# Performance work log

Measured on AMD Instinct MI355X. Metric: run time of the kernel, lower is better.

## Reference

```python
import jax, jax.numpy as jnp
import numpy as np

N_NODES = 100000
N_EDGES = 1600000
DIM_IN, DIM_H, DIM_OUT = 500, 64, 8


def setup_inputs() -> dict:
    key = jax.random.key(0)
    k_x, k_e, k_w1, k_w2 = jax.random.split(key, 4)
    x = jax.random.normal(k_x, (N_NODES, DIM_IN), dtype=jnp.float32)
    edge_index = jax.random.randint(k_e, (2, N_EDGES), 0, N_NODES, dtype=jnp.int32)
    # Glorot-ish init for linear weights, zero bias (PyG GCNConv default)
    W1 = jax.random.normal(k_w1, (DIM_IN, DIM_H), dtype=jnp.float32) * (1.0 / np.sqrt(DIM_IN))
    b1 = jnp.zeros((DIM_H,), dtype=jnp.float32)
    W2 = jax.random.normal(k_w2, (DIM_H, DIM_OUT), dtype=jnp.float32) * (1.0 / np.sqrt(DIM_H))
    b2 = jnp.zeros((DIM_OUT,), dtype=jnp.float32)
    return {"x": x, "edge_index": edge_index, "W1": W1, "b1": b1, "W2": W2, "b2": b2}


def _gcn_conv(h, W, b, src, dst, edge_norm, num_nodes):
    """GCNConv: out = D^{-1/2}(A+I)D^{-1/2} (h W) + b, via gather/scatter over edges."""
    hw = h @ W                                  # [N, d_out] dense transform
    msg = hw[src] * edge_norm[:, None]          # [E+N, d_out] gather + scale
    agg = jax.ops.segment_sum(msg, dst, num_segments=num_nodes)  # scatter-add
    return agg + b


def reference(x, edge_index, W1, b1, W2, b2):
    num_nodes = x.shape[0]
    # Add self-loops (PyG GCNConv default: add_self_loops=True)
    loops = jnp.arange(num_nodes, dtype=edge_index.dtype)
    src = jnp.concatenate([edge_index[0], loops])
    dst = jnp.concatenate([edge_index[1], loops])
    # Symmetric normalization from in-degree of loop-augmented graph
    deg = jax.ops.segment_sum(jnp.ones_like(dst, dtype=x.dtype), dst,
                              num_segments=num_nodes)
    dinv = jnp.where(deg > 0, jax.lax.rsqrt(deg), 0.0)
    edge_norm = dinv[src] * dinv[dst]           # [E+N]
    # Eval-mode forward (dropout is identity when not training)
    h = jax.nn.relu(_gcn_conv(x, W1, b1, src, dst, edge_norm, num_nodes))
    h = _gcn_conv(h, W2, b2, src, dst, edge_norm, num_nodes)
    return jax.nn.log_softmax(h, axis=1)
```

## Files before the change

kernel.cpp:

```cpp
#include <hip/hip_runtime.h>
#include <stdint.h>

#define NN 100000
#define NE 1600000
#define DIN 500
#define DH 64
#define DOUT 8
#define KP 512
#define MAXDEG 64

#define FILL_EPT 4
#define FILL_PASSES 16
#define FILL_RS ((NN + FILL_PASSES - 1) / FILL_PASSES)

typedef __attribute__((ext_vector_type(8))) short short8;
typedef __attribute__((ext_vector_type(4))) float f32x4;
typedef unsigned short ushort_t;

static __device__ __forceinline__ ushort_t f2bf(float f) {
  union { float f; uint32_t u; } v; v.f = f;
  uint32_t u = v.u;
  return (ushort_t)((u + 0x7FFFu + ((u >> 16) & 1u)) >> 16);
}
static __device__ __forceinline__ float bf2f(ushort_t h) {
  union { uint32_t u; float f; } v; v.u = ((uint32_t)h) << 16;
  return v.f;
}

static __device__ __forceinline__ void gload16(const void* g, void* l) {
  __builtin_amdgcn_global_load_lds((const __attribute__((address_space(1))) uint32_t*)g,
                                   (__attribute__((address_space(3))) uint32_t*)l, 16, 0, 0);
}

__global__ __launch_bounds__(256) void k_fill(const int* __restrict__ ei,
                                              int* __restrict__ cursor,
                                              int* __restrict__ colsrc) {
  int t = blockIdx.x * 256 + threadIdx.x;
  const int T = gridDim.x * 256;
  int s[FILL_EPT], d[FILL_EPT];
#pragma unroll
  for (int k = 0; k < FILL_EPT; ++k) {
    int id = t + k * T;
    s[k] = 0; d[k] = -1;
    if (id < NE) { s[k] = ei[id]; d[k] = ei[NE + id]; }
    else if (id < NE + NN) { s[k] = id - NE; d[k] = s[k]; }
  }
#pragma unroll 1
  for (int p = 0; p < FILL_PASSES; ++p) {
    int lo = p * FILL_RS;
    int hi = lo + FILL_RS;
#pragma unroll
    for (int k = 0; k < FILL_EPT; ++k) {
      bool act = (d[k] >= lo) && (d[k] < hi);
      if (__any(act)) {
        if (act) {
          int pos = atomicAdd(&cursor[d[k]], 1);
          if (pos < MAXDEG) colsrc[d[k] * MAXDEG + pos] = s[k];
        }
      }
    }
  }
}

__global__ __launch_bounds__(256) void k_dinv(const int* __restrict__ cursor,
                                              float* __restrict__ dinv) {
  int v = blockIdx.x * 256 + threadIdx.x;
  if (v >= NN) return;
  dinv[v] = 1.0f / sqrtf((float)cursor[v]);
}

__global__ __launch_bounds__(256) void k_w1cvt(const float* __restrict__ W1,
                                               ushort_t* __restrict__ bt) {
  int id = blockIdx.x * 256 + threadIdx.x;
  if (id >= DH * KP * 2) return;
  int i = id & 7, lane = (id >> 3) & 63, h = (id >> 9) & 1;
  int off = (id >> 10) & 3, kkg = id >> 12;
  int r = lane & 15, g = lane >> 4;
  int col = off * 16 + r;
  int k = kkg * 32 + g * 8 + i;
  float v = (k < DIN) ? W1[k * DH + col] : 0.0f;
  ushort_t hi = f2bf(v);
  bt[id] = h ? f2bf(v - bf2f(hi)) : hi;
}

__global__ __launch_bounds__(256) void k_gemm1(const float* __restrict__ x,
                                               const ushort_t* __restrict__ bt,
                                               ushort_t* __restrict__ hwb) {
  __shared__ float lds[2][64 * 128];
  int tid = threadIdx.x;
  int lane = tid & 63, w = tid >> 6;
  int r = lane & 15, g = lane >> 4;
  int row0 = blockIdx.x * 64;

  auto stage = [&](int ch, int b) {
    float* base = &lds[b][0];
#pragma unroll
    for (int j = 0; j < 8; ++j) {
      int idx = j * 256 + tid;
      int row = idx >> 5;
      int q   = idx & 31;
      int qd  = q ^ (row & 7);
      int kq  = ch * 32 + qd;
      if (kq > 124) kq = 124;
      int grow = row0 + row;
      if (grow >= NN) grow = NN - 1;
      gload16(x + (size_t)grow * DIN + kq * 4, base + idx * 4);
    }
  };

  f32x4 acc0 = {0,0,0,0}, acc1 = {0,0,0,0}, acc2 = {0,0,0,0}, acc3 = {0,0,0,0};
  int rowl = w * 16 + r;
  int sw = rowl & 7;

  stage(0, 0);
  __syncthreads();
#pragma unroll 1
  for (int ch = 0; ch < 4; ++ch) {
    if (ch < 3) stage(ch + 1, (ch + 1) & 1);
    __builtin_amdgcn_sched_barrier(0);
#pragma unroll
    for (int kk = 0; kk < 4; ++kk) {
      int q0 = kk * 8 + g * 2;
      f32x4 v0 = *(const f32x4*)(&lds[ch & 1][rowl * 128 + ((q0)     ^ sw) * 4]);
      f32x4 v1 = *(const f32x4*)(&lds[ch & 1][rowl * 128 + ((q0 + 1) ^ sw) * 4]);
      float a[8] = {v0.x, v0.y, v0.z, v0.w, v1.x, v1.y, v1.z, v1.w};
      short8 ah, al;
#pragma unroll
      for (int i = 0; i < 8; ++i) {
        ushort_t hi = f2bf(a[i]);
        ah[i] = (short)hi;
        al[i] = (short)f2bf(a[i] - bf2f(hi));
      }
      int kkg = ch * 4 + kk;
      const ushort_t* bph = bt + (size_t)(kkg * 4 * 2) * 512 + lane * 8;
#define TILE(T, OFF)                                                            \
      {                                                                         \
        short8 bhf = *(const short8*)(bph + (OFF) * 2 * 512);                   \
        short8 blf = *(const short8*)(bph + ((OFF) * 2 + 1) * 512);             \
        T = __builtin_amdgcn_mfma_f32_16x16x32_bf16(ah, bhf, T, 0, 0, 0);       \
        T = __builtin_amdgcn_mfma_f32_16x16x32_bf16(al, bhf, T, 0, 0, 0);       \
        T = __builtin_amdgcn_mfma_f32_16x16x32_bf16(ah, blf, T, 0, 0, 0);       \
      }
      TILE(acc0, 0) TILE(acc1, 1) TILE(acc2, 2) TILE(acc3, 3)
#undef TILE
    }
    __syncthreads();
  }
  int wrow0 = row0 + w * 16;
#pragma unroll
  for (int i = 0; i < 4; ++i) {
    int orow = wrow0 + g * 4 + i;
    if (orow < NN) {
      ushort_t* o = hwb + (size_t)orow * DH + r;
      o[0]  = f2bf(acc0[i]);
      o[16] = f2bf(acc1[i]);
      o[32] = f2bf(acc2[i]);
      o[48] = f2bf(acc3[i]);
    }
  }
}

__global__ __launch_bounds__(256) void k_agg1(const ushort_t* __restrict__ hwb,
                                              const int* __restrict__ colsrc,
                                              const int* __restrict__ cnt,
                                              const float* __restrict__ dinv,
                                              const float* __restrict__ b1,
                                              const float* __restrict__ W2,
                                              float* __restrict__ hw2) {
  int lane = threadIdx.x & 63;
  int v = blockIdx.x * 4 + (threadIdx.x >> 6);
  if (v >= NN) return;
  int c = cnt[v]; if (c > MAXDEG) c = MAXDEG;
  float dv = dinv[v];
  const int* cl = colsrc + v * MAXDEG;
  int si = cl[lane];
  bool act = lane < c;
  if (!act) si = 0;
  float nrmv = act ? dinv[si] * dv : 0.0f;
  float acc = 0.0f;
  for (int i0 = 0; i0 < c; i0 += 16) {
    float val[16];
#pragma unroll
    for (int j = 0; j < 16; ++j) {
      int s = __builtin_amdgcn_readlane(si, i0 + j);
      val[j] = bf2f(hwb[(size_t)s * DH + lane]);
    }
#pragma unroll
    for (int j = 0; j < 16; ++j) {
      float nrm = __uint_as_float(__builtin_amdgcn_readlane(__float_as_uint(nrmv), i0 + j));
      acc = fmaf(val[j], nrm, acc);
    }
  }
  float h = acc + b1[lane];
  h = h > 0.0f ? h : 0.0f;
  const float* w2r = W2 + lane * DOUT;
  float p0 = h * w2r[0], p1 = h * w2r[1], p2 = h * w2r[2], p3 = h * w2r[3];
  float p4 = h * w2r[4], p5 = h * w2r[5], p6 = h * w2r[6], p7 = h * w2r[7];
#pragma unroll
  for (int off = 32; off > 0; off >>= 1) {
    p0 += __shfl_xor(p0, off); p1 += __shfl_xor(p1, off);
    p2 += __shfl_xor(p2, off); p3 += __shfl_xor(p3, off);
    p4 += __shfl_xor(p4, off); p5 += __shfl_xor(p5, off);
    p6 += __shfl_xor(p6, off); p7 += __shfl_xor(p7, off);
  }
  if (lane == 0) {
    float4 q0 = {p0, p1, p2, p3}, q1 = {p4, p5, p6, p7};
    *(float4*)(hw2 + (size_t)v * DOUT)     = q0;
    *(float4*)(hw2 + (size_t)v * DOUT + 4) = q1;
  }
}

__global__ __launch_bounds__(256) void k_agg2(const float* __restrict__ hw2,
                                              const int* __restrict__ colsrc,
                                              const int* __restrict__ cnt,
                                              const float* __restrict__ dinv,
                                              const float* __restrict__ b2,
                                              float* __restrict__ out) {
  int lane = threadIdx.x & 63;
  int v = blockIdx.x * 4 + (threadIdx.x >> 6);
  if (v >= NN) return;
  int e = lane >> 3, f = lane & 7;
  int c = cnt[v]; if (c > MAXDEG) c = MAXDEG;
  float dv = dinv[v];
  const int* cl = colsrc + v * MAXDEG;
  float acc = 0.0f;
  for (int i0 = 0; i0 < c; i0 += 8) {
    int i = i0 + e;
    bool a2 = i < c;
    int s = a2 ? cl[i] : 0;
    float nrm = a2 ? dinv[s] * dv : 0.0f;
    float val = hw2[(size_t)s * DOUT + f] * nrm;
    val += __shfl_xor(val, 8);
    val += __shfl_xor(val, 16);
    val += __shfl_xor(val, 32);
    acc += val;
  }
  acc += b2[f];
  float m = acc;
  m = fmaxf(m, __shfl_xor(m, 1));
  m = fmaxf(m, __shfl_xor(m, 2));
  m = fmaxf(m, __shfl_xor(m, 4));
  float ex = expf(acc - m);
  float sum = ex;
  sum += __shfl_xor(sum, 1);
  sum += __shfl_xor(sum, 2);
  sum += __shfl_xor(sum, 4);
  float ls = m + logf(sum);
  if (e == 0) out[(size_t)v * DOUT + f] = acc - ls;
}

extern "C" void kernel_launch(void* const* d_in, const int* in_sizes, int n_in,
                              void* d_out, int out_size, void* d_ws, size_t ws_size,
                              hipStream_t stream) {
  const float* x  = (const float*)d_in[0];
  const int*   ei = (const int*)d_in[1];
  const float* W1 = (const float*)d_in[2];
  const float* b1 = (const float*)d_in[3];
  const float* W2 = (const float*)d_in[4];
  const float* b2 = (const float*)d_in[5];
  float* out = (float*)d_out;

  char* w = (char*)d_ws;
  size_t off = 0;
  auto alloc = [&](size_t bytes) {
    char* p = w + off;
    off += (bytes + 255) & ~(size_t)255;
    return (void*)p;
  };
  int*      cursor = (int*)alloc((size_t)NN * 4);
  float*    dinv   = (float*)alloc((size_t)NN * 4);
  ushort_t* bt     = (ushort_t*)alloc((size_t)DH * KP * 2 * 2);
  int*      colsrc = (int*)alloc((size_t)NN * MAXDEG * 4);
  ushort_t* hwb    = (ushort_t*)alloc((size_t)NN * DH * 2);
  float*    hw2    = (float*)alloc((size_t)NN * DOUT * 4);

  hipMemsetAsync(cursor, 0, (size_t)NN * 4, stream);
  int fill_blocks = (NE + NN + 256 * FILL_EPT - 1) / (256 * FILL_EPT);
  k_fill<<<fill_blocks, 256, 0, stream>>>(ei, cursor, colsrc);
  k_dinv<<<(NN + 255) / 256, 256, 0, stream>>>(cursor, dinv);
  k_w1cvt<<<(DH * KP * 2 + 255) / 256, 256, 0, stream>>>(W1, bt);
  k_gemm1<<<(NN + 63) / 64, 256, 0, stream>>>(x, bt, hwb);
  k_agg1<<<(NN + 3) / 4, 256, 0, stream>>>(hwb, colsrc, cursor, dinv, b1, W2, hw2);
  k_agg2<<<(NN + 3) / 4, 256, 0, stream>>>(hw2, colsrc, cursor, dinv, b2, out);
}
```

Before: 286.7 us.

## Fuse CSR fill and GEMM1 into one interleaved kernel, prefetch B fragments

Merges the atomic-based CSR fill and the first dense GEMM into one launch whose blocks alternate between fill and GEMM roles, so the latency-bound scatter atomics overlap with the bandwidth/MFMA-bound GEMM. The GEMM now double-buffers the W1 bf16 fragments in registers ahead of each MFMA step and drops the LDS XOR swizzle. It also adds nontemporal loads for edges and a nontemporal output store. Risks include more LDS bank conflicts without the swizzle, higher register pressure from 16 short8 buffers, and fill blocks reserving the full LDS allocation.

```diff
diff --git a/kernel.cpp b/kernel.cpp
--- a/kernel.cpp
+++ b/kernel.cpp
@@ -12,6 +12,8 @@
 #define FILL_EPT 4
 #define FILL_PASSES 16
 #define FILL_RS ((NN + FILL_PASSES - 1) / FILL_PASSES)
+#define GEMMB ((NN + 63) / 64)
+#define FILLB ((NE + NN + 256 * FILL_EPT - 1) / (256 * FILL_EPT))
 
 typedef __attribute__((ext_vector_type(8))) short short8;
 typedef __attribute__((ext_vector_type(4))) float f32x4;
@@ -30,36 +32,6 @@
 static __device__ __forceinline__ void gload16(const void* g, void* l) {
   __builtin_amdgcn_global_load_lds((const __attribute__((address_space(1))) uint32_t*)g,
                                    (__attribute__((address_space(3))) uint32_t*)l, 16, 0, 0);
-}
-
-__global__ __launch_bounds__(256) void k_fill(const int* __restrict__ ei,
-                                              int* __restrict__ cursor,
-                                              int* __restrict__ colsrc) {
-  int t = blockIdx.x * 256 + threadIdx.x;
-  const int T = gridDim.x * 256;
-  int s[FILL_EPT], d[FILL_EPT];
-#pragma unroll
-  for (int k = 0; k < FILL_EPT; ++k) {
-    int id = t + k * T;
-    s[k] = 0; d[k] = -1;
-    if (id < NE) { s[k] = ei[id]; d[k] = ei[NE + id]; }
-    else if (id < NE + NN) { s[k] = id - NE; d[k] = s[k]; }
-  }
-#pragma unroll 1
-  for (int p = 0; p < FILL_PASSES; ++p) {
-    int lo = p * FILL_RS;
-    int hi = lo + FILL_RS;
-#pragma unroll
-    for (int k = 0; k < FILL_EPT; ++k) {
-      bool act = (d[k] >= lo) && (d[k] < hi);
-      if (__any(act)) {
-        if (act) {
-          int pos = atomicAdd(&cursor[d[k]], 1);
-          if (pos < MAXDEG) colsrc[d[k] * MAXDEG + pos] = s[k];
-        }
-      }
-    }
-  }
 }
 
 __global__ __launch_bounds__(256) void k_dinv(const int* __restrict__ cursor,
@@ -83,67 +55,111 @@
   bt[id] = h ? f2bf(v - bf2f(hi)) : hi;
 }
 
-__global__ __launch_bounds__(256) void k_gemm1(const float* __restrict__ x,
+__global__ __launch_bounds__(256) void k_front(const int* __restrict__ ei,
+                                               int* __restrict__ cursor,
+                                               int* __restrict__ colsrc,
+                                               const float* __restrict__ x,
                                                const ushort_t* __restrict__ bt,
                                                ushort_t* __restrict__ hwb) {
   __shared__ float lds[2][64 * 128];
+  int bid = blockIdx.x;
   int tid = threadIdx.x;
+
+  int fid, gid;
+  if (bid < 2 * GEMMB) {
+    if ((bid & 1) == 0) { fid = bid >> 1; gid = -1; }
+    else                { gid = bid >> 1; fid = -1; }
+  } else { fid = GEMMB + (bid - 2 * GEMMB); gid = -1; }
+
+  if (fid >= 0) {
+    int t = fid * 256 + tid;
+    const int T = FILLB * 256;
+    int s[FILL_EPT], d[FILL_EPT];
+#pragma unroll
+    for (int k = 0; k < FILL_EPT; ++k) {
+      int id = t + k * T;
+      s[k] = 0; d[k] = -1;
+      if (id < NE) {
+        s[k] = __builtin_nontemporal_load(ei + id);
+        d[k] = __builtin_nontemporal_load(ei + NE + id);
+      } else if (id < NE + NN) { s[k] = id - NE; d[k] = s[k]; }
+    }
+#pragma unroll 1
+    for (int p = 0; p < FILL_PASSES; ++p) {
+      int lo = p * FILL_RS;
+      int hi = lo + FILL_RS;
+#pragma unroll
+      for (int k = 0; k < FILL_EPT; ++k) {
+        bool act = (d[k] >= lo) && (d[k] < hi);
+        if (__any(act)) {
+          if (act) {
+            int pos = atomicAdd(&cursor[d[k]], 1);
+            if (pos < MAXDEG) colsrc[d[k] * MAXDEG + pos] = s[k];
+          }
+        }
+      }
+    }
+    return;
+  }
+
   int lane = tid & 63, w = tid >> 6;
   int r = lane & 15, g = lane >> 4;
-  int row0 = blockIdx.x * 64;
+  int row0 = gid * 64;
+  int rowl = w * 16 + r;
 
   auto stage = [&](int ch, int b) {
     float* base = &lds[b][0];
 #pragma unroll
     for (int j = 0; j < 8; ++j) {
       int idx = j * 256 + tid;
-      int row = idx >> 5;
-      int q   = idx & 31;
-      int qd  = q ^ (row & 7);
-      int kq  = ch * 32 + qd;
-      if (kq > 124) kq = 124;
-      int grow = row0 + row;
-      if (grow >= NN) grow = NN - 1;
+      int row = idx >> 5, q = idx & 31;
+      int kq = ch * 32 + q; if (kq > 124) kq = 124;
+      int grow = row0 + row; if (grow >= NN) grow = NN - 1;
       gload16(x + (size_t)grow * DIN + kq * 4, base + idx * 4);
     }
   };
 
+  short8 Bc[8], Bn[8];
+  auto loadB = [&](short8* B, int kkg) {
+    const ushort_t* bp = bt + (size_t)kkg * 8 * 512 + lane * 8;
+#pragma unroll
+    for (int u = 0; u < 8; ++u) B[u] = *(const short8*)(bp + u * 512);
+  };
+
   f32x4 acc0 = {0,0,0,0}, acc1 = {0,0,0,0}, acc2 = {0,0,0,0}, acc3 = {0,0,0,0};
-  int rowl = w * 16 + r;
-  int sw = rowl & 7;
-
+
+  auto compute = [&](int ch, int kk, const short8* B) {
+    const float* lp = &lds[ch & 1][rowl * 128 + (kk * 8 + g * 2) * 4];
+    f32x4 v0 = *(const f32x4*)lp;
+    f32x4 v1 = *(const f32x4*)(lp + 4);
+    float a[8] = {v0.x, v0.y, v0.z, v0.w, v1.x, v1.y, v1.z, v1.w};
+    short8 ah, al;
+#pragma unroll
+    for (int i = 0; i < 8; ++i) {
+      ushort_t hi = f2bf(a[i]);
+      ah[i] = (short)hi;
+      al[i] = (short)f2bf(a[i] - bf2f(hi));
+    }
+#define TILE(T, OFF)                                                          \
+    T = __builtin_amdgcn_mfma_f32_16x16x32_bf16(ah, B[(OFF)*2],   T, 0, 0, 0);\
+    T = __builtin_amdgcn_mfma_f32_16x16x32_bf16(al, B[(OFF)*2],   T, 0, 0, 0);\
+    T = __builtin_amdgcn_mfma_f32_16x16x32_bf16(ah, B[(OFF)*2+1], T, 0, 0, 0);
+    TILE(acc0, 0) TILE(acc1, 1) TILE(acc2, 2) TILE(acc3, 3)
+#undef TILE
+  };
+
+  loadB(Bc, 0);
   stage(0, 0);
   __syncthreads();
 #pragma unroll 1
   for (int ch = 0; ch < 4; ++ch) {
     if (ch < 3) stage(ch + 1, (ch + 1) & 1);
-    __builtin_amdgcn_sched_barrier(0);
-#pragma unroll
-    for (int kk = 0; kk < 4; ++kk) {
-      int q0 = kk * 8 + g * 2;
-      f32x4 v0 = *(const f32x4*)(&lds[ch & 1][rowl * 128 + ((q0)     ^ sw) * 4]);
-      f32x4 v1 = *(const f32x4*)(&lds[ch & 1][rowl * 128 + ((q0 + 1) ^ sw) * 4]);
-      float a[8] = {v0.x, v0.y, v0.z, v0.w, v1.x, v1.y, v1.z, v1.w};
-      short8 ah, al;
-#pragma unroll
-      for (int i = 0; i < 8; ++i) {
-        ushort_t hi = f2bf(a[i]);
-        ah[i] = (short)hi;
-        al[i] = (short)f2bf(a[i] - bf2f(hi));
-      }
-      int kkg = ch * 4 + kk;
-      const ushort_t* bph = bt + (size_t)(kkg * 4 * 2) * 512 + lane * 8;
-#define TILE(T, OFF)                                                            \
-      {                                                                         \
-        short8 bhf = *(const short8*)(bph + (OFF) * 2 * 512);                   \
-        short8 blf = *(const short8*)(bph + ((OFF) * 2 + 1) * 512);             \
-        T = __builtin_amdgcn_mfma_f32_16x16x32_bf16(ah, bhf, T, 0, 0, 0);       \
-        T = __builtin_amdgcn_mfma_f32_16x16x32_bf16(al, bhf, T, 0, 0, 0);       \
-        T = __builtin_amdgcn_mfma_f32_16x16x32_bf16(ah, blf, T, 0, 0, 0);       \
-      }
-      TILE(acc0, 0) TILE(acc1, 1) TILE(acc2, 2) TILE(acc3, 3)
-#undef TILE
-    }
+    int k0 = ch * 4;
+    loadB(Bn, k0 + 1);  compute(ch, 0, Bc);
+    loadB(Bc, k0 + 2);  compute(ch, 1, Bn);
+    loadB(Bn, k0 + 3);  compute(ch, 2, Bc);
+    if (ch < 3) loadB(Bc, k0 + 4);
+    compute(ch, 3, Bn);
     __syncthreads();
   }
   int wrow0 = row0 + w * 16;
@@ -246,7 +262,7 @@
   sum += __shfl_xor(sum, 2);
   sum += __shfl_xor(sum, 4);
   float ls = m + logf(sum);
-  if (e == 0) out[(size_t)v * DOUT + f] = acc - ls;
+  if (e == 0) __builtin_nontemporal_store(acc - ls, &out[(size_t)v * DOUT + f]);
 }
 
 extern "C" void kernel_launch(void* const* d_in, const int* in_sizes, int n_in,
@@ -275,11 +291,9 @@
   float*    hw2    = (float*)alloc((size_t)NN * DOUT * 4);
 
   hipMemsetAsync(cursor, 0, (size_t)NN * 4, stream);
-  int fill_blocks = (NE + NN + 256 * FILL_EPT - 1) / (256 * FILL_EPT);
-  k_fill<<<fill_blocks, 256, 0, stream>>>(ei, cursor, colsrc);
+  k_w1cvt<<<(DH * KP * 2 + 255) / 256, 256, 0, stream>>>(W1, bt);
+  k_front<<<2 * GEMMB + (FILLB - GEMMB), 256, 0, stream>>>(ei, cursor, colsrc, x, bt, hwb);
   k_dinv<<<(NN + 255) / 256, 256, 0, stream>>>(cursor, dinv);
-  k_w1cvt<<<(DH * KP * 2 + 255) / 256, 256, 0, stream>>>(W1, bt);
-  k_gemm1<<<(NN + 63) / 64, 256, 0, stream>>>(x, bt, hwb);
   k_agg1<<<(NN + 3) / 4, 256, 0, stream>>>(hwb, colsrc, cursor, dinv, b1, W2, hw2);
   k_agg2<<<(NN + 3) / 4, 256, 0, stream>>>(hw2, colsrc, cursor, dinv, b2, out);
 }
```

After: 300.5 us. +4.8%, slower.

## Restructure GEMM1 to stage full-K row chunks and keep W1 tiles in registers

Applied to the files above, without the earlier changes.

The first-layer GEMM now stages 16 full rows of x (all 500 floats) per chunk as one contiguous global-to-LDS copy, replacing the earlier K-sliced, swizzled staging. Each wave owns one 16-column output tile and preloads its split-bf16 W1 fragments into registers once, so B is no longer re-read from global memory inside the loop. Output is written after each row chunk. In exchange it uses many more VGPRs (launch bounds set to 2 blocks per SM), the row stride of 500 may cause LDS bank conflicts, and the K padding reads past row ends and possibly into uninitialised LDS, relying on the zero-padded W1 rows.

```diff
diff --git a/kernel.cpp b/kernel.cpp
--- a/kernel.cpp
+++ b/kernel.cpp
@@ -8,10 +8,12 @@
 #define DOUT 8
 #define KP 512
 #define MAXDEG 64
+#define MAXQ (NN * 125)
 
 #define FILL_EPT 4
 #define FILL_PASSES 16
 #define FILL_RS ((NN + FILL_PASSES - 1) / FILL_PASSES)
+#define GEMMB ((NN + 63) / 64)
 
 typedef __attribute__((ext_vector_type(8))) short short8;
 typedef __attribute__((ext_vector_type(4))) float f32x4;
@@ -83,46 +85,49 @@
   bt[id] = h ? f2bf(v - bf2f(hi)) : hi;
 }
 
-__global__ __launch_bounds__(256) void k_gemm1(const float* __restrict__ x,
-                                               const ushort_t* __restrict__ bt,
-                                               ushort_t* __restrict__ hwb) {
-  __shared__ float lds[2][64 * 128];
+__global__ __launch_bounds__(256, 2) void k_gemm1(const float* __restrict__ x,
+                                                  const ushort_t* __restrict__ bt,
+                                                  ushort_t* __restrict__ hwb) {
+  __shared__ float lds[2][8016];
   int tid = threadIdx.x;
   int lane = tid & 63, w = tid >> 6;
   int r = lane & 15, g = lane >> 4;
   int row0 = blockIdx.x * 64;
 
-  auto stage = [&](int ch, int b) {
+  short8 Ball[32];
+#pragma unroll
+  for (int kkg = 0; kkg < 16; ++kkg) {
+    const ushort_t* bp = bt + (size_t)((kkg * 4 + w) * 2) * 512 + lane * 8;
+    Ball[kkg * 2]     = *(const short8*)bp;
+    Ball[kkg * 2 + 1] = *(const short8*)(bp + 512);
+  }
+
+  auto stage = [&](int c, int b) {
     float* base = &lds[b][0];
+    int q0 = (row0 + c * 16) * 125;
 #pragma unroll
     for (int j = 0; j < 8; ++j) {
       int idx = j * 256 + tid;
-      int row = idx >> 5;
-      int q   = idx & 31;
-      int qd  = q ^ (row & 7);
-      int kq  = ch * 32 + qd;
-      if (kq > 124) kq = 124;
-      int grow = row0 + row;
-      if (grow >= NN) grow = NN - 1;
-      gload16(x + (size_t)grow * DIN + kq * 4, base + idx * 4);
+      if (idx < 2000) {
+        int q = q0 + idx;
+        if (q >= MAXQ) q = MAXQ - 1;
+        gload16(x + (size_t)q * 4, base + idx * 4);
+      }
     }
   };
-
-  f32x4 acc0 = {0,0,0,0}, acc1 = {0,0,0,0}, acc2 = {0,0,0,0}, acc3 = {0,0,0,0};
-  int rowl = w * 16 + r;
-  int sw = rowl & 7;
 
   stage(0, 0);
   __syncthreads();
 #pragma unroll 1
-  for (int ch = 0; ch < 4; ++ch) {
-    if (ch < 3) stage(ch + 1, (ch + 1) & 1);
+  for (int c = 0; c < 4; ++c) {
+    if (c < 3) stage(c + 1, (c + 1) & 1);
     __builtin_amdgcn_sched_barrier(0);
-#pragma unroll
-    for (int kk = 0; kk < 4; ++kk) {
-      int q0 = kk * 8 + g * 2;
-      f32x4 v0 = *(const f32x4*)(&lds[ch & 1][rowl * 128 + ((q0)     ^ sw) * 4]);
-      f32x4 v1 = *(const f32x4*)(&lds[ch & 1][rowl * 128 + ((q0 + 1) ^ sw) * 4]);
+    f32x4 acc = {0, 0, 0, 0};
+#pragma unroll
+    for (int kkg = 0; kkg < 16; ++kkg) {
+      const float* lp = &lds[c & 1][r * 500 + kkg * 32 + g * 8];
+      f32x4 v0 = *(const f32x4*)lp;
+      f32x4 v1 = *(const f32x4*)(lp + 4);
       float a[8] = {v0.x, v0.y, v0.z, v0.w, v1.x, v1.y, v1.z, v1.w};
       short8 ah, al;
 #pragma unroll
@@ -131,32 +136,17 @@
         ah[i] = (short)hi;
         al[i] = (short)f2bf(a[i] - bf2f(hi));
       }
-      int kkg = ch * 4 + kk;
-      const ushort_t* bph = bt + (size_t)(kkg * 4 * 2) * 512 + lane * 8;
-#define TILE(T, OFF)                                                            \
-      {                                                                         \
-        short8 bhf = *(const short8*)(bph + (OFF) * 2 * 512);                   \
-        short8 blf = *(const short8*)(bph + ((OFF) * 2 + 1) * 512);             \
-        T = __builtin_amdgcn_mfma_f32_16x16x32_bf16(ah, bhf, T, 0, 0, 0);       \
-        T = __builtin_amdgcn_mfma_f32_16x16x32_bf16(al, bhf, T, 0, 0, 0);       \
-        T = __builtin_amdgcn_mfma_f32_16x16x32_bf16(ah, blf, T, 0, 0, 0);       \
-      }
-      TILE(acc0, 0) TILE(acc1, 1) TILE(acc2, 2) TILE(acc3, 3)
-#undef TILE
+      acc = __builtin_amdgcn_mfma_f32_16x16x32_bf16(ah, Ball[kkg * 2],     acc, 0, 0, 0);
+      acc = __builtin_amdgcn_mfma_f32_16x16x32_bf16(al, Ball[kkg * 2],     acc, 0, 0, 0);
+      acc = __builtin_amdgcn_mfma_f32_16x16x32_bf16(ah, Ball[kkg * 2 + 1], acc, 0, 0, 0);
+    }
+    int crow0 = row0 + c * 16;
+#pragma unroll
+    for (int i = 0; i < 4; ++i) {
+      int orow = crow0 + g * 4 + i;
+      if (orow < NN) hwb[(size_t)orow * DH + w * 16 + r] = f2bf(acc[i]);
     }
     __syncthreads();
-  }
-  int wrow0 = row0 + w * 16;
-#pragma unroll
-  for (int i = 0; i < 4; ++i) {
-    int orow = wrow0 + g * 4 + i;
-    if (orow < NN) {
-      ushort_t* o = hwb + (size_t)orow * DH + r;
-      o[0]  = f2bf(acc0[i]);
-      o[16] = f2bf(acc1[i]);
-      o[32] = f2bf(acc2[i]);
-      o[48] = f2bf(acc3[i]);
-    }
   }
 }
 
@@ -279,7 +269,7 @@
   k_fill<<<fill_blocks, 256, 0, stream>>>(ei, cursor, colsrc);
   k_dinv<<<(NN + 255) / 256, 256, 0, stream>>>(cursor, dinv);
   k_w1cvt<<<(DH * KP * 2 + 255) / 256, 256, 0, stream>>>(W1, bt);
-  k_gemm1<<<(NN + 63) / 64, 256, 0, stream>>>(x, bt, hwb);
+  k_gemm1<<<GEMMB, 256, 0, stream>>>(x, bt, hwb);
   k_agg1<<<(NN + 3) / 4, 256, 0, stream>>>(hwb, colsrc, cursor, dinv, b1, W2, hw2);
   k_agg2<<<(NN + 3) / 4, 256, 0, stream>>>(hw2, colsrc, cursor, dinv, b2, out);
 }
```

Result: faster. 265.0 us (-7.6%).
